# Optimization experiments

Hardware: AMD Instinct MI355X
Metric: run time of the kernel (lower is better)

The kernel has to match this reference:

```python
import jax, jax.numpy as jnp
import numpy as np

B, T, DIM = 2, 2048, 1024
H, DH, E, K = 16, 64, 8, 2


def setup_inputs() -> dict:
    key = jax.random.key(0)
    ks = jax.random.split(key, 7)
    s = 0.02
    return {
        "x":  jax.random.normal(ks[0], (B, T, DIM), jnp.float32),
        "Wq": jax.random.normal(ks[1], (H, DH, DIM), jnp.float32) * s,  # Linear(dim -> h*dh), reshaped
        "Wk": jax.random.normal(ks[2], (H, DH, DIM), jnp.float32) * s,
        "Wv": jax.random.normal(ks[3], (E, DH, DIM), jnp.float32) * s,  # per-expert Linear(dim -> dh)
        "Ws": jax.random.normal(ks[4], (H, E, DIM), jnp.float32) * s,   # V-gate Linear(dim -> h*e)
        "Wd": jax.random.normal(ks[5], (H, E, DIM), jnp.float32) * s,   # O-gate Linear(dim -> h*e)
        "Wo": jax.random.normal(ks[6], (E, DIM, DH), jnp.float32) * s,  # per-expert Linear(dh -> dim)
    }


def reference(x, Wq, Wk, Wv, Ws, Wd, Wo):
    scale = DH ** -0.5
    # projections: [b,h,t,dh]
    q = jnp.einsum('btc,hdc->bhtd', x, Wq)
    k = jnp.einsum('btc,hdc->bhtd', x, Wk)

    # ---- compute_moe (V experts): top-k gate, sigmoid weights ----
    gate_v = jnp.einsum('btc,hec->bthe', x, Ws)              # [b,t,h,e]
    w, sel = jax.lax.top_k(gate_v, K)                        # [b,t,h,K]
    wsig = jax.nn.sigmoid(w)
    oh = jax.nn.one_hot(sel, E, dtype=x.dtype)               # [b,t,h,K,e]
    mix_v = jnp.einsum('bthk,bthke->bthe', wsig, oh)         # weighted routing mask
    proj_v = jnp.einsum('btc,edc->bted', x, Wv)              # all-expert V projections (E small)
    v = jnp.einsum('bthe,bted->bhtd', mix_v, proj_v)         # [b,h,t,dh]

    # ---- standard attention core ----
    scores = jnp.einsum('bhid,bhjd->bhij', q * scale, k)     # [b,h,t,t]
    probs = jax.nn.softmax(scores, axis=-1)
    attn = jnp.einsum('bhij,bhjd->bihd', probs, v)           # [b,t,h,dh]

    # ---- compute_moe_o (O experts): top-k gate; NOTE original never uses its
    # softmax weights, so selected experts are summed UNWEIGHTED ----
    gate_o = jnp.einsum('btc,hec->bthe', x, Wd)
    _, sel_o = jax.lax.top_k(gate_o, K)
    mask_o = jax.nn.one_hot(sel_o, E, dtype=x.dtype).sum(axis=3)  # [b,t,h,e] in {0,1}
    res = jnp.einsum('bthe,bthd,efd->bthf', mask_o, attn, Wo)     # [b,t,h,dim]
    return res.sum(axis=2)                                        # [b,t,dim]
```

## Files before the change

kernel.cpp:

```cpp
#include <hip/hip_runtime.h>
#include <math.h>

#define TSEQ 2048
#define NB   2
#define NH   16
#define NE   8
#define DHD  64
#define MDIM 1024
#define MBT  4096
#define LDQKV 2560
#define GTAU 1e-3f
#define MAXFLAG 16384

typedef __attribute__((ext_vector_type(8))) short bf16x8;
typedef __attribute__((ext_vector_type(4))) float f32x4;
typedef __attribute__((ext_vector_type(16))) float f32x16;
typedef unsigned int u32;

__device__ inline unsigned short f2bf(float f) {
    union { float f; unsigned u; } v; v.f = f;
    unsigned r = v.u + 0x7fff + ((v.u >> 16) & 1);
    return (unsigned short)(r >> 16);
}
__device__ inline float bf2f(unsigned short h) {
    union { unsigned u; float f; } v; v.u = ((unsigned)h) << 16;
    return v.f;
}
__device__ inline u32 cvtpk(float a, float b) {
    u32 r;
    asm("v_cvt_pk_bf16_f32 %0, %1, %2" : "=v"(r) : "v"(a), "v"(b));
    return r;
}
__device__ inline float fexp2(float x) {
#if __has_builtin(__builtin_amdgcn_exp2f)
    return __builtin_amdgcn_exp2f(x);
#else
    float r; asm("v_exp_f32 %0, %1" : "=v"(r) : "v"(x)); return r;
#endif
}

__device__ inline void gload16(const void* g, void* l) {
    __builtin_amdgcn_global_load_lds((const __attribute__((address_space(1))) u32*)g,
                                     (__attribute__((address_space(3))) u32*)l, 16, 0, 0);
}

__device__ inline void cast8s(const float* __restrict__ in, unsigned short* __restrict__ out,
                              int i, float sc) {
    const float4* p = (const float4*)(in + (size_t)i * 8);
    float4 a = p[0], b = p[1];
    unsigned short o[8] = { f2bf(a.x*sc), f2bf(a.y*sc), f2bf(a.z*sc), f2bf(a.w*sc),
                            f2bf(b.x*sc), f2bf(b.y*sc), f2bf(b.z*sc), f2bf(b.w*sc) };
    *(uint4*)(out + (size_t)i * 8) = *(const uint4*)o;
}
__device__ inline void cast8hl(const float* __restrict__ in,
                               unsigned short* __restrict__ oh, unsigned short* __restrict__ ol,
                               int i) {
    const float4* p = (const float4*)(in + (size_t)i * 8);
    float4 a = p[0], b = p[1];
    float f[8] = { a.x, a.y, a.z, a.w, b.x, b.y, b.z, b.w };
    unsigned short h8[8], l8[8];
    #pragma unroll
    for (int j = 0; j < 8; ++j) {
        unsigned short hi = f2bf(f[j]);
        h8[j] = hi;
        l8[j] = f2bf(f[j] - bf2f(hi));
    }
    *(uint4*)(oh + (size_t)i * 8) = *(const uint4*)h8;
    *(uint4*)(ol + (size_t)i * 8) = *(const uint4*)l8;
}

__global__ __launch_bounds__(256)
void prep(const float* __restrict__ x,  const float* __restrict__ Wq,
          const float* __restrict__ Wk, const float* __restrict__ Wv,
          const float* __restrict__ Ws, const float* __restrict__ Wd,
          const float* __restrict__ Wo,
          unsigned short* __restrict__ xb, unsigned short* __restrict__ xbl,
          unsigned short* __restrict__ Wqkvb,
          unsigned short* __restrict__ Wsdh, unsigned short* __restrict__ Wsdl,
          unsigned short* __restrict__ WoTh, unsigned short* __restrict__ WoTl,
          u32* __restrict__ flags)
{
    const float qsc = 0.125f * 1.4426950408889634f;
    int b = blockIdx.x, tid = threadIdx.x;
    if (b == 0 && tid == 0) flags[0] = 0;
    if (b < 2048)      cast8hl(x, xb, xbl,          (b        ) * 256 + tid);
    else if (b < 2560) cast8s(Wq, Wqkvb,            (b - 2048) * 256 + tid, qsc);
    else if (b < 3072) cast8s(Wk, Wqkvb + 1048576,  (b - 2560) * 256 + tid, 1.f);
    else if (b < 3328) cast8s(Wv, Wqkvb + 2097152,  (b - 3072) * 256 + tid, 1.f);
    else if (b < 3456) {
        int i = (b - 3328) * 256 + tid;
        const float* src = (i < 16384) ? Ws + (size_t)i * 8 : Wd + (size_t)(i - 16384) * 8;
        const float4* p = (const float4*)src;
        float4 a = p[0], bq = p[1];
        float f8[8] = { a.x, a.y, a.z, a.w, bq.x, bq.y, bq.z, bq.w };
        unsigned short h8[8], l8[8];
        #pragma unroll
        for (int j = 0; j < 8; ++j) {
            unsigned short hi = f2bf(f8[j]);
            h8[j] = hi;
            l8[j] = f2bf(f8[j] - bf2f(hi));
        }
        *(uint4*)(Wsdh + (size_t)i * 8) = *(const uint4*)h8;
        *(uint4*)(Wsdl + (size_t)i * 8) = *(const uint4*)l8;
    } else {
        int idx = (b - 3456) * 256 + tid;
        int f = idx >> 9, ed = idx & 511, e = ed >> 6, d = ed & 63;
        float v = Wo[(size_t)e * (MDIM * DHD) + (size_t)f * DHD + d];
        unsigned short hi = f2bf(v);
        WoTh[idx] = hi;
        WoTl[idx] = f2bf(v - bf2f(hi));
    }
}

__global__ __launch_bounds__(256)
void qkvgate(const unsigned short* __restrict__ A,
             const unsigned short* __restrict__ B,
             unsigned short* __restrict__ C,
             const unsigned short* __restrict__ Al,
             const unsigned short* __restrict__ Bh2, const unsigned short* __restrict__ Bl2,
             float* __restrict__ Gf)
{
    __shared__ __align__(16) unsigned short S[8192];
    const int tid = threadIdx.x;
    const int lane = tid & 63, wave = tid >> 6;
    const int fr = lane & 15, fg = lane >> 4;
    const int grow = lane >> 2, gcol = (lane & 3) * 8;

    if (blockIdx.x < 640) {
        const int K = 1024, N = LDQKV, nbx = 20;
        unsigned short* As = S;
        unsigned short* Bs = S + 4096;
        const int o = blockIdx.x;
        const int virt = (o & 7) * 80 + (o >> 3);
        const int bx = virt % nbx, by = virt / nbx;
        const int m0 = by * 128, n0 = bx * 128;
        const int wm = (wave >> 1) * 64, wn = (wave & 1) * 64;

        f32x4 acc[4][4];
        #pragma unroll
        for (int i = 0; i < 4; ++i)
            #pragma unroll
            for (int j = 0; j < 4; ++j) acc[i][j] = (f32x4)0.f;

        for (int k0 = 0; k0 < K; k0 += 32) {
            __syncthreads();
            const unsigned short* gA = A + (size_t)(m0 + wave * 32 + grow) * K + k0 + gcol;
            gload16(gA,                  As + wave * 1024);
            gload16(gA + (size_t)16 * K, As + wave * 1024 + 512);
            const unsigned short* gB = B + (size_t)(n0 + wave * 32 + grow) * K + k0 + gcol;
            gload16(gB,                  Bs + wave * 1024);
            gload16(gB + (size_t)16 * K, Bs + wave * 1024 + 512);
            __syncthreads();
            bf16x8 af[4], bfr[4];
            #pragma unroll
            for (int t = 0; t < 4; ++t) {
                af[t]  = *(const bf16x8*)(As + (wm + t * 16 + fr) * 32 + fg * 8);
                bfr[t] = *(const bf16x8*)(Bs + (wn + t * 16 + fr) * 32 + fg * 8);
            }
            #pragma unroll
            for (int i = 0; i < 4; ++i)
                #pragma unroll
                for (int j = 0; j < 4; ++j)
                    acc[i][j] = __builtin_amdgcn_mfma_f32_16x16x32_bf16(af[i], bfr[j], acc[i][j], 0, 0, 0);
        }
        #pragma unroll
        for (int i = 0; i < 4; ++i)
            #pragma unroll
            for (int j = 0; j < 4; ++j)
                #pragma unroll
                for (int rr = 0; rr < 4; ++rr) {
                    int row = m0 + wm + i * 16 + fg * 4 + rr;
                    int col = n0 + wn + j * 16 + fr;
                    C[(size_t)row * N + col] = f2bf(acc[i][j][rr]);
                }
    } else {
        const int K = 1024, N = 256;
        const int g = blockIdx.x - 640;
        const int m0 = (g >> 2) * 64, n0 = (g & 3) * 64;
        const int wm = (wave >> 1) * 32, wn = (wave & 1) * 32;
        const unsigned short* src = (wave == 0) ? A : (wave == 1) ? Al : (wave == 2) ? Bh2 : Bl2;
        const int brow = (wave >= 2) ? n0 : m0;

        f32x4 acc[2][2];
        #pragma unroll
        for (int i = 0; i < 2; ++i)
            #pragma unroll
            for (int j = 0; j < 2; ++j) acc[i][j] = (f32x4)0.f;

        for (int k0 = 0; k0 < K; k0 += 32) {
            __syncthreads();
            #pragma unroll
            for (int i = 0; i < 4; ++i)
                gload16(src + (size_t)(brow + i * 16 + grow) * K + k0 + gcol,
                        S + wave * 2048 + i * 512);
            __syncthreads();
            bf16x8 ah[2], al[2], bh[2], bl[2];
            #pragma unroll
            for (int t = 0; t < 2; ++t) {
                ah[t] = *(const bf16x8*)(S +        (wm + t * 16 + fr) * 32 + fg * 8);
                al[t] = *(const bf16x8*)(S + 2048 + (wm + t * 16 + fr) * 32 + fg * 8);
                bh[t] = *(const bf16x8*)(S + 4096 + (wn + t * 16 + fr) * 32 + fg * 8);
                bl[t] = *(const bf16x8*)(S + 6144 + (wn + t * 16 + fr) * 32 + fg * 8);
            }
            #pragma unroll
            for (int i = 0; i < 2; ++i)
                #pragma unroll
                for (int j = 0; j < 2; ++j) {
                    acc[i][j] = __builtin_amdgcn_mfma_f32_16x16x32_bf16(ah[i], bh[j], acc[i][j], 0, 0, 0);
                    acc[i][j] = __builtin_amdgcn_mfma_f32_16x16x32_bf16(ah[i], bl[j], acc[i][j], 0, 0, 0);
                    acc[i][j] = __builtin_amdgcn_mfma_f32_16x16x32_bf16(al[i], bh[j], acc[i][j], 0, 0, 0);
                }
        }
        #pragma unroll
        for (int i = 0; i < 2; ++i)
            #pragma unroll
            for (int j = 0; j < 2; ++j)
                #pragma unroll
                for (int rr = 0; rr < 4; ++rr) {
                    int row = m0 + wm + i * 16 + fg * 4 + rr;
                    int col = n0 + wn + j * 16 + fr;
                    Gf[(size_t)row * N + col] = acc[i][j][rr];
                }
    }
}

__global__ __launch_bounds__(256)
void mfma_gemm3(const unsigned short* __restrict__ Ah, const unsigned short* __restrict__ Al,
                const unsigned short* __restrict__ Bh, const unsigned short* __restrict__ Bl,
                float* __restrict__ C)
{
    const int Kc = 512, N = 1024;
    __shared__ __align__(16) unsigned short Ash[128 * 32];
    __shared__ __align__(16) unsigned short Asl[128 * 32];
    __shared__ __align__(16) unsigned short Bsh[128 * 32];
    __shared__ __align__(16) unsigned short Bsl[128 * 32];
    const int o = blockIdx.x;
    const int virt = (o & 7) * 32 + (o >> 3);
    const int bx = virt & 7, by = virt >> 3;
    const int tid = threadIdx.x;
    const int lane = tid & 63, wave = tid >> 6;
    const int m0 = by * 128, n0 = bx * 128;
    const int wm = (wave >> 1) * 64, wn = (wave & 1) * 64;
    const int fr = lane & 15, fg = lane >> 4;
    const int grow = lane >> 2, gcol = (lane & 3) * 8;

    f32x4 acc[4][4];
    #pragma unroll
    for (int i = 0; i < 4; ++i)
        #pragma unroll
        for (int j = 0; j < 4; ++j) acc[i][j] = (f32x4)0.f;

    for (int k0 = 0; k0 < Kc; k0 += 32) {
        __syncthreads();
        const size_t roff  = (size_t)(m0 + wave * 32 + grow) * Kc + k0 + gcol;
        const size_t roffB = (size_t)(n0 + wave * 32 + grow) * Kc + k0 + gcol;
        gload16(Ah + roff,             Ash + wave * 1024);
        gload16(Ah + roff + 16 * Kc,   Ash + wave * 1024 + 512);
        gload16(Al + roff,             Asl + wave * 1024);
        gload16(Al + roff + 16 * Kc,   Asl + wave * 1024 + 512);
        gload16(Bh + roffB,            Bsh + wave * 1024);
        gload16(Bh + roffB + 16 * Kc,  Bsh + wave * 1024 + 512);
        gload16(Bl + roffB,            Bsl + wave * 1024);
        gload16(Bl + roffB + 16 * Kc,  Bsl + wave * 1024 + 512);
        __syncthreads();
        bf16x8 ah[4], al[4], bh[4], bl[4];
        #pragma unroll
        for (int t = 0; t < 4; ++t) {
            ah[t] = *(const bf16x8*)(Ash + (wm + t * 16 + fr) * 32 + fg * 8);
            al[t] = *(const bf16x8*)(Asl + (wm + t * 16 + fr) * 32 + fg * 8);
            bh[t] = *(const bf16x8*)(Bsh + (wn + t * 16 + fr) * 32 + fg * 8);
            bl[t] = *(const bf16x8*)(Bsl + (wn + t * 16 + fr) * 32 + fg * 8);
        }
        #pragma unroll
        for (int i = 0; i < 4; ++i)
            #pragma unroll
            for (int j = 0; j < 4; ++j) {
                acc[i][j] = __builtin_amdgcn_mfma_f32_16x16x32_bf16(ah[i], bh[j], acc[i][j], 0, 0, 0);
                acc[i][j] = __builtin_amdgcn_mfma_f32_16x16x32_bf16(ah[i], bl[j], acc[i][j], 0, 0, 0);
                acc[i][j] = __builtin_amdgcn_mfma_f32_16x16x32_bf16(al[i], bh[j], acc[i][j], 0, 0, 0);
            }
    }
    #pragma unroll
    for (int i = 0; i < 4; ++i)
        #pragma unroll
        for (int j = 0; j < 4; ++j)
            #pragma unroll
            for (int rr = 0; rr < 4; ++rr) {
                int row = m0 + wm + i * 16 + fg * 4 + rr;
                int col = n0 + wn + j * 16 + fr;
                C[(size_t)row * N + col] = acc[i][j][rr];
            }
}

__global__ __launch_bounds__(256)
void gate_topk2(const float* __restrict__ Gf,
                float2* __restrict__ wv, u32* __restrict__ selv, u32* __restrict__ selo,
                u32* __restrict__ flags)
{
    int item = blockIdx.x * 256 + threadIdx.x;
    int bt = item >> 4, h = item & 15;
    const float* g = Gf + (size_t)bt * 256 + h * NE;
    float b1 = -1e30f, b2 = -1e30f, b3 = -1e30f; int e1 = 0, e2 = 0;
    #pragma unroll
    for (int e = 0; e < NE; ++e) {
        float v = g[e];
        if (v > b1)      { b3 = b2; b2 = b1; e2 = e1; b1 = v; e1 = e; }
        else if (v > b2) { b3 = b2; b2 = v;  e2 = e; }
        else if (v > b3) { b3 = v; }
    }
    wv[item] = make_float2(1.f / (1.f + __expf(-b1)), 1.f / (1.f + __expf(-b2)));
    selv[item] = (u32)e1 | ((u32)e2 << 4);
    if (b2 - b3 < GTAU) {
        u32 p = atomicAdd(flags, 1u);
        if (p < MAXFLAG) flags[1 + p] = (u32)item;
    }
    const float* go = g + 128;
    float o1 = -1e30f, o2 = -1e30f, o3 = -1e30f; int f1 = 0, f2 = 0;
    #pragma unroll
    for (int e = 0; e < NE; ++e) {
        float v = go[e];
        if (v > o1)      { o3 = o2; o2 = o1; f2 = f1; o1 = v; f1 = e; }
        else if (v > o2) { o3 = o2; o2 = v;  f2 = e; }
        else if (v > o3) { o3 = v; }
    }
    selo[item] = (1u << f1) | (1u << f2);
    if (o2 - o3 < GTAU) {
        u32 p = atomicAdd(flags, 1u);
        if (p < MAXFLAG) flags[1 + p] = (u32)item | 0x10000u;
    }
}

__global__ __launch_bounds__(256)
void gate_fix(const float* __restrict__ x, const float* __restrict__ Ws,
              const float* __restrict__ Wd, const u32* __restrict__ flags,
              float2* __restrict__ wv, u32* __restrict__ selv, u32* __restrict__ selo)
{
    u32 nf = flags[0]; if (nf > MAXFLAG) nf = MAXFLAG;
    int gw = (blockIdx.x * 256 + threadIdx.x) >> 6;
    int lane = threadIdx.x & 63;
    int nwaves = gridDim.x * 4;
    for (u32 w = gw; w < nf; w += nwaves) {
        u32 rec = flags[1 + w];
        int item = rec & 0xffff, which = rec >> 16;
        int bt = item >> 4, h = item & 15;
        const float* W = (which ? Wd : Ws) + (size_t)h * NE * MDIM + lane * 16;
        const float* xr = x + (size_t)bt * MDIM + lane * 16;
        double g[8];
        #pragma unroll
        for (int e = 0; e < 8; ++e) {
            double s = 0.0;
            #pragma unroll
            for (int c = 0; c < 16; ++c)
                s += (double)xr[c] * (double)W[(size_t)e * MDIM + c];
            g[e] = s;
        }
        #pragma unroll
        for (int off = 32; off; off >>= 1)
            #pragma unroll
            for (int e = 0; e < 8; ++e)
                g[e] += __shfl_xor(g[e], off, 64);
        if (lane == 0) {
            double b1 = -1e300, b2 = -1e300; int i1 = 0, i2 = 0;
            #pragma unroll
            for (int e = 0; e < 8; ++e) {
                double v = g[e];
                if (v > b1)      { b2 = b1; i2 = i1; b1 = v; i1 = e; }
                else if (v > b2) { b2 = v;  i2 = e; }
            }
            if (which == 0) {
                wv[item] = make_float2(1.f / (1.f + __expf(-(float)b1)),
                                       1.f / (1.f + __expf(-(float)b2)));
                selv[item] = (u32)i1 | ((u32)i2 << 4);
            } else {
                selo[item] = (1u << i1) | (1u << i2);
            }
        }
    }
}

#define VTP 72
__global__ __launch_bounds__(256)
void vtrans(const unsigned short* __restrict__ QKVb, const float2* __restrict__ wv,
            const u32* __restrict__ selv, unsigned short* __restrict__ Vtg)
{
    __shared__ __align__(16) unsigned short Ls[256 * VTP];
    const int vid = blockIdx.x;
    const int xcd = vid & 7, local = vid >> 3;
    const int virt = xcd * 32 + local;
    const int b = virt >> 7, rem = virt & 127;
    const int tblk = rem >> 4, h = rem & 15;
    const int tid = threadIdx.x;

    {
        const int bt = b * TSEQ + tblk * 256 + tid;
        u32 s = selv[bt * 16 + h];
        float2 w = wv[bt * 16 + h];
        int e1 = s & 15, e2 = (s >> 4) & 15;
        const unsigned short* pv = QKVb + (size_t)bt * LDQKV + 2048;
        #pragma unroll
        for (int c = 0; c < 8; ++c) {
            uint4 a  = *(const uint4*)(pv + e1 * 64 + c * 8);
            uint4 bb = *(const uint4*)(pv + e2 * 64 + c * 8);
            unsigned short ea[8], eb[8], eo[8];
            *(uint4*)ea = a; *(uint4*)eb = bb;
            #pragma unroll
            for (int j = 0; j < 8; ++j)
                eo[j] = f2bf(w.x * bf2f(ea[j]) + w.y * bf2f(eb[j]));
            *(uint4*)(Ls + tid * VTP + c * 8) = *(const uint4*)eo;
        }
    }
    __syncthreads();
    {
        const int d = tid & 63, outer = tid >> 6;
        const size_t vrow = ((size_t)((b * NH + h) * DHD + d)) * TSEQ + tblk * 256;
        #pragma unroll
        for (int c8 = 0; c8 < 8; ++c8) {
            int t0 = (outer * 8 + c8) * 8;
            unsigned short o[8];
            #pragma unroll
            for (int j = 0; j < 8; ++j)
                o[j] = Ls[(t0 + j) * VTP + d];
            *(uint4*)(Vtg + vrow + t0) = *(const uint4*)o;
        }
    }
}

#define SPA 72
#define MFMA32(A,B,C) __builtin_amdgcn_mfma_f32_32x32x16_bf16(A, B, C, 0, 0, 0)
__global__ __launch_bounds__(256)
void attn_mfma(const unsigned short* __restrict__ QKVb,
               const unsigned short* __restrict__ Vtg,
               float* __restrict__ Op0, float* __restrict__ Op1,
               float* __restrict__ lp)
{
    __shared__ __align__(16) unsigned short Ks[64 * SPA];
    __shared__ __align__(16) unsigned short Vt[64 * SPA];
    const int vid = blockIdx.x;
    const int xcd = vid & 7, sl = vid >> 3;
    const int grp = xcd * 8 + (sl >> 4);
    const int q0  = (sl & 15) * 128;
    const int h   = grp & 15;
    const int z   = grp >> 4;
    const int b = z >> 1, split = z & 1;
    const int tid = threadIdx.x;
    const int lane = tid & 63, wq = tid >> 6;
    const int ql = lane & 31;
    const int hi = lane >> 5;
    const size_t base_q = ((size_t)b * TSEQ) * LDQKV + h * DHD;
    const size_t base_k = base_q + 1024;
    const size_t base_v = ((size_t)(b * NH + h) * DHD) * TSEQ;
    const int k00 = split * 1024;

    const int qrow = q0 + wq * 32 + ql;
    bf16x8 qa[4];
    #pragma unroll
    for (int t = 0; t < 4; ++t)
        qa[t] = *(const bf16x8*)(QKVb + base_q + (size_t)qrow * LDQKV + t * 16 + hi * 8);

    f32x16 o0 = (f32x16)0.f, o1 = (f32x16)0.f;
    float l_lane = 0.f;

    const int srow = tid >> 2, scol = (tid & 3) * 8;
    uint4 kr0 = *(const uint4*)(QKVb + base_k + (size_t)(k00 + srow) * LDQKV + scol);
    uint4 kr1 = *(const uint4*)(QKVb + base_k + (size_t)(k00 + srow) * LDQKV + scol + 32);
    uint4 vr0 = *(const uint4*)(Vtg + base_v + (size_t)srow * TSEQ + k00 + scol);
    uint4 vr1 = *(const uint4*)(Vtg + base_v + (size_t)srow * TSEQ + k00 + scol + 32);

    const int NT = 1024 / 64;
    for (int kb = 0; kb < NT; ++kb) {
        __syncthreads();
        *(uint4*)(Ks + srow * SPA + scol)      = kr0;
        *(uint4*)(Ks + srow * SPA + scol + 32) = kr1;
        *(uint4*)(Vt + srow * SPA + scol)      = vr0;
        *(uint4*)(Vt + srow * SPA + scol + 32) = vr1;
        __syncthreads();
        if (kb + 1 < NT) {
            const size_t gk = base_k + (size_t)(k00 + (kb + 1) * 64 + srow) * LDQKV + scol;
            const size_t gv = base_v + (size_t)srow * TSEQ + k00 + (kb + 1) * 64 + scol;
            kr0 = *(const uint4*)(QKVb + gk);
            kr1 = *(const uint4*)(QKVb + gk + 32);
            vr0 = *(const uint4*)(Vtg + gv);
            vr1 = *(const uint4*)(Vtg + gv + 32);
        }
        f32x16 s0 = (f32x16)0.f, s1 = (f32x16)0.f;
        #pragma unroll
        for (int t = 0; t < 4; ++t) {
            bf16x8 k0 = *(const bf16x8*)(Ks + ql * SPA + t * 16 + hi * 8);
            bf16x8 k1 = *(const bf16x8*)(Ks + (32 + ql) * SPA + t * 16 + hi * 8);
            s0 = MFMA32(k0, qa[t], s0);
            s1 = MFMA32(k1, qa[t], s1);
        }
        float ls0 = 0.f, ls1 = 0.f;
        u32 w[8];
        #pragma unroll
        for (int r = 0; r < 16; r += 2) {
            float pa = fexp2(s0[r]), pb = fexp2(s0[r + 1]);
            s0[r] = pa; s0[r + 1] = pb;
            ls0 += pa; ls1 += pb;
        }
        #pragma unroll
        for (int m = 0; m < 8; ++m) w[m] = cvtpk(s0[2*m], s0[2*m+1]);
        #pragma unroll
        for (int tl = 0; tl < 2; ++tl) {
            const int mb = 4 * tl, tk = tl;
            u32 send0 = hi ? w[mb]   : w[mb+2];
            u32 send1 = hi ? w[mb+1] : w[mb+3];
            u32 r0 = (u32)__shfl_xor((int)send0, 32, 64);
            u32 r1 = (u32)__shfl_xor((int)send1, 32, 64);
            union { u32 uw[4]; bf16x8 v; } pu;
            pu.uw[0] = hi ? r0 : w[mb];
            pu.uw[1] = hi ? r1 : w[mb+1];
            pu.uw[2] = hi ? w[mb+2] : r0;
            pu.uw[3] = hi ? w[mb+3] : r1;
            bf16x8 v0 = *(const bf16x8*)(Vt + ql * SPA + tk * 16 + hi * 8);
            bf16x8 v1 = *(const bf16x8*)(Vt + (32 + ql) * SPA + tk * 16 + hi * 8);
            o0 = MFMA32(pu.v, v0, o0);
            o1 = MFMA32(pu.v, v1, o1);
        }
        #pragma unroll
        for (int r = 0; r < 16; r += 2) {
            float pa = fexp2(s1[r]), pb = fexp2(s1[r + 1]);
            s1[r] = pa; s1[r + 1] = pb;
            ls0 += pa; ls1 += pb;
        }
        #pragma unroll
        for (int m = 0; m < 8; ++m) w[m] = cvtpk(s1[2*m], s1[2*m+1]);
        #pragma unroll
        for (int tl = 0; tl < 2; ++tl) {
            const int mb = 4 * tl, tk = 2 + tl;
            u32 send0 = hi ? w[mb]   : w[mb+2];
            u32 send1 = hi ? w[mb+1] : w[mb+3];
            u32 r0 = (u32)__shfl_xor((int)send0, 32, 64);
            u32 r1 = (u32)__shfl_xor((int)send1, 32, 64);
            union { u32 uw[4]; bf16x8 v; } pu;
            pu.uw[0] = hi ? r0 : w[mb];
            pu.uw[1] = hi ? r1 : w[mb+1];
            pu.uw[2] = hi ? w[mb+2] : r0;
            pu.uw[3] = hi ? w[mb+3] : r1;
            bf16x8 v0 = *(const bf16x8*)(Vt + ql * SPA + tk * 16 + hi * 8);
            bf16x8 v1 = *(const bf16x8*)(Vt + (32 + ql) * SPA + tk * 16 + hi * 8);
            o0 = MFMA32(pu.v, v0, o0);
            o1 = MFMA32(pu.v, v1, o1);
        }
        l_lane += ls0 + ls1;
    }
    float l_tot = l_lane + __shfl_xor(l_lane, 32, 64);
    float* Op = split ? Op1 : Op0;
    const size_t ob = ((size_t)b * TSEQ) * MDIM + h * DHD;
    #pragma unroll
    for (int r = 0; r < 16; ++r) {
        int qr = q0 + wq * 32 + (r & 3) + 8 * (r >> 2) + 4 * hi;
        Op[ob + (size_t)qr * MDIM + ql]      = o0[r];
        Op[ob + (size_t)qr * MDIM + 32 + ql] = o1[r];
    }
    if (hi == 0)
        lp[(((size_t)split * NB + b) * NH + h) * TSEQ + q0 + wq * 32 + ql] = l_tot;
}

__global__ __launch_bounds__(256)
void compute_U2(const float* __restrict__ Op0, const float* __restrict__ Op1,
                const float* __restrict__ lp, const u32* __restrict__ selo,
                unsigned short* __restrict__ Uh, unsigned short* __restrict__ Ul)
{
    int t = blockIdx.x * 256 + threadIdx.x;
    int bt = t >> 6, d = t & 63;
    int b = bt >> 11, ts = bt & 2047;
    float att[16];
    #pragma unroll
    for (int h = 0; h < NH; ++h) {
        size_t li = ((size_t)b * NH + h) * TSEQ + ts;
        float l = lp[li] + lp[li + (size_t)NB * NH * TSEQ];
        size_t oi = (size_t)bt * MDIM + h * DHD + d;
        att[h] = (Op0[oi] + Op1[oi]) / l;
    }
    const u32* sp = selo + bt * 16;
    u32 m[16];
    #pragma unroll
    for (int h = 0; h < NH; ++h) m[h] = sp[h];
    #pragma unroll
    for (int e = 0; e < NE; ++e) {
        float sum = 0.f;
        #pragma unroll
        for (int h = 0; h < NH; ++h)
            if (m[h] & (1u << e)) sum += att[h];
        int idx = bt * 512 + e * 64 + d;
        unsigned short hi16 = f2bf(sum);
        Uh[idx] = hi16;
        Ul[idx] = f2bf(sum - bf2f(hi16));
    }
}

extern "C" void kernel_launch(void* const* d_in, const int* in_sizes, int n_in,
                              void* d_out, int out_size, void* d_ws, size_t ws_size,
                              hipStream_t stream)
{
    const float* x  = (const float*)d_in[0];
    const float* Wq = (const float*)d_in[1];
    const float* Wk = (const float*)d_in[2];
    const float* Wv = (const float*)d_in[3];
    const float* Ws = (const float*)d_in[4];
    const float* Wd = (const float*)d_in[5];
    const float* Wo = (const float*)d_in[6];
    float* out = (float*)d_out;
    char* ws = (char*)d_ws;

    unsigned short* xb    = (unsigned short*)(ws);
    unsigned short* Wqkvb = (unsigned short*)(ws + 8388608);
    float*          Op0   = (float*)(ws);
    unsigned short* QKVb  = (unsigned short*)(ws + 16777216);
    unsigned short* Vtg   = (unsigned short*)(ws + 37748736);
    unsigned short* xbl   = (unsigned short*)(ws + 46137344);
    float*          Op1   = (float*)(ws + 46137344);
    float*          lp    = (float*)(ws + 62914560);
    unsigned short* WoTh  = (unsigned short*)(ws + 63438848);
    unsigned short* WoTl  = (unsigned short*)(ws + 64487424);
    float*          Gf    = (float*)(ws + 65536000);
    unsigned short* Uh    = (unsigned short*)(ws + 65536000);
    u32*            flags = (u32*)(ws + 69730304);
    unsigned short* Ul    = (unsigned short*)(ws + 69730304);
    float2*         wvp   = (float2*)(ws + 73924608);
    u32*            selv  = (u32*)(ws + 74448896);
    u32*            selo  = (u32*)(ws + 74711040);
    unsigned short* Wsdh  = (unsigned short*)(ws + 74973184);
    unsigned short* Wsdl  = (unsigned short*)(ws + 75497472);

    dim3 blk(256);
    prep<<<5504, blk, 0, stream>>>(x, Wq, Wk, Wv, Ws, Wd, Wo,
                                   xb, xbl, Wqkvb, Wsdh, Wsdl, WoTh, WoTl, flags);

    qkvgate<<<896, blk, 0, stream>>>(xb, Wqkvb, QKVb, xbl, Wsdh, Wsdl, Gf);

    gate_topk2<<<256, blk, 0, stream>>>(Gf, wvp, selv, selo, flags);
    gate_fix<<<128, blk, 0, stream>>>(x, Ws, Wd, flags, wvp, selv, selo);

    vtrans<<<256, blk, 0, stream>>>(QKVb, wvp, selv, Vtg);

    attn_mfma<<<1024, blk, 0, stream>>>(QKVb, Vtg, Op0, Op1, lp);

    compute_U2<<<1024, blk, 0, stream>>>(Op0, Op1, lp, selo, Uh, Ul);
    mfma_gemm3<<<256, blk, 0, stream>>>(Uh, Ul, WoTh, WoTl, out);
}
```

Measured before the change: 167.6 us.

## Fuse gate top-k into gate GEMM epilogue and halve output GEMM N-tile

The gate GEMM blocks inside qkvgate now stage their 64x64 fp32 tile in shared memory and run the top-2 expert selection, sigmoid weights and near-tie flagging directly. This removes the gate_topk2 launch and the Gf round trip through global memory. Separately, the final output GEMM uses 128x64 tiles instead of 128x128, doubling the grid to 512 blocks for better CU occupancy at the cost of reloading the A operand for twice as many tiles.

New measurement: 156.5 us. -6.6%, faster.

```diff
diff --git a/kernel.cpp b/kernel.cpp
--- a/kernel.cpp
+++ b/kernel.cpp
@@ -118,7 +118,8 @@
              unsigned short* __restrict__ C,
              const unsigned short* __restrict__ Al,
              const unsigned short* __restrict__ Bh2, const unsigned short* __restrict__ Bl2,
-             float* __restrict__ Gf)
+             float2* __restrict__ wv, u32* __restrict__ selv, u32* __restrict__ selo,
+             u32* __restrict__ flags)
 {
     __shared__ __align__(16) unsigned short S[8192];
     const int tid = threadIdx.x;
@@ -174,7 +175,7 @@
                     C[(size_t)row * N + col] = f2bf(acc[i][j][rr]);
                 }
     } else {
-        const int K = 1024, N = 256;
+        const int K = 1024;
         const int g = blockIdx.x - 640;
         const int m0 = (g >> 2) * 64, n0 = (g & 3) * 64;
         const int wm = (wave >> 1) * 32, wn = (wave & 1) * 32;
@@ -211,16 +212,47 @@
                     acc[i][j] = __builtin_amdgcn_mfma_f32_16x16x32_bf16(al[i], bh[j], acc[i][j], 0, 0, 0);
                 }
         }
+        float* Tf = (float*)S;
+        __syncthreads();
         #pragma unroll
         for (int i = 0; i < 2; ++i)
             #pragma unroll
             for (int j = 0; j < 2; ++j)
                 #pragma unroll
-                for (int rr = 0; rr < 4; ++rr) {
-                    int row = m0 + wm + i * 16 + fg * 4 + rr;
-                    int col = n0 + wn + j * 16 + fr;
-                    Gf[(size_t)row * N + col] = acc[i][j][rr];
+                for (int rr = 0; rr < 4; ++rr)
+                    Tf[(wm + i * 16 + fg * 4 + rr) * 64 + wn + j * 16 + fr] = acc[i][j][rr];
+        __syncthreads();
+        const int type = (n0 >= 128);
+        const int hbase = (n0 & 127) >> 3;
+        #pragma unroll
+        for (int k = 0; k < 2; ++k) {
+            int it = tid + k * 256;
+            int lr = it >> 3, lh = it & 7;
+            int item = (m0 + lr) * 16 + hbase + lh;
+            const float* gp = Tf + lr * 64 + lh * 8;
+            float b1 = -1e30f, b2 = -1e30f, b3 = -1e30f; int e1 = 0, e2 = 0;
+            #pragma unroll
+            for (int e = 0; e < NE; ++e) {
+                float v = gp[e];
+                if (v > b1)      { b3 = b2; b2 = b1; e2 = e1; b1 = v; e1 = e; }
+                else if (v > b2) { b3 = b2; b2 = v;  e2 = e; }
+                else if (v > b3) { b3 = v; }
+            }
+            if (type == 0) {
+                wv[item] = make_float2(1.f / (1.f + __expf(-b1)), 1.f / (1.f + __expf(-b2)));
+                selv[item] = (u32)e1 | ((u32)e2 << 4);
+                if (b2 - b3 < GTAU) {
+                    u32 p = atomicAdd(flags, 1u);
+                    if (p < MAXFLAG) flags[1 + p] = (u32)item;
                 }
+            } else {
+                selo[item] = (1u << e1) | (1u << e2);
+                if (b2 - b3 < GTAU) {
+                    u32 p = atomicAdd(flags, 1u);
+                    if (p < MAXFLAG) flags[1 + p] = (u32)item | 0x10000u;
+                }
+            }
+        }
     }
 }
 
@@ -232,49 +264,50 @@
     const int Kc = 512, N = 1024;
     __shared__ __align__(16) unsigned short Ash[128 * 32];
     __shared__ __align__(16) unsigned short Asl[128 * 32];
-    __shared__ __align__(16) unsigned short Bsh[128 * 32];
-    __shared__ __align__(16) unsigned short Bsl[128 * 32];
+    __shared__ __align__(16) unsigned short Bsh[64 * 32];
+    __shared__ __align__(16) unsigned short Bsl[64 * 32];
     const int o = blockIdx.x;
-    const int virt = (o & 7) * 32 + (o >> 3);
-    const int bx = virt & 7, by = virt >> 3;
+    const int virt = (o & 7) * 64 + (o >> 3);
+    const int bx = virt & 15, by = virt >> 4;
     const int tid = threadIdx.x;
     const int lane = tid & 63, wave = tid >> 6;
-    const int m0 = by * 128, n0 = bx * 128;
-    const int wm = (wave >> 1) * 64, wn = (wave & 1) * 64;
+    const int m0 = by * 128, n0 = bx * 64;
+    const int wm = (wave >> 1) * 64, wn = (wave & 1) * 32;
     const int fr = lane & 15, fg = lane >> 4;
     const int grow = lane >> 2, gcol = (lane & 3) * 8;
 
-    f32x4 acc[4][4];
+    f32x4 acc[4][2];
     #pragma unroll
     for (int i = 0; i < 4; ++i)
         #pragma unroll
-        for (int j = 0; j < 4; ++j) acc[i][j] = (f32x4)0.f;
+        for (int j = 0; j < 2; ++j) acc[i][j] = (f32x4)0.f;
 
     for (int k0 = 0; k0 < Kc; k0 += 32) {
         __syncthreads();
         const size_t roff  = (size_t)(m0 + wave * 32 + grow) * Kc + k0 + gcol;
-        const size_t roffB = (size_t)(n0 + wave * 32 + grow) * Kc + k0 + gcol;
+        const size_t roffB = (size_t)(n0 + wave * 16 + grow) * Kc + k0 + gcol;
         gload16(Ah + roff,             Ash + wave * 1024);
         gload16(Ah + roff + 16 * Kc,   Ash + wave * 1024 + 512);
         gload16(Al + roff,             Asl + wave * 1024);
         gload16(Al + roff + 16 * Kc,   Asl + wave * 1024 + 512);
-        gload16(Bh + roffB,            Bsh + wave * 1024);
-        gload16(Bh + roffB + 16 * Kc,  Bsh + wave * 1024 + 512);
-        gload16(Bl + roffB,            Bsl + wave * 1024);
-        gload16(Bl + roffB + 16 * Kc,  Bsl + wave * 1024 + 512);
+        gload16(Bh + roffB,            Bsh + wave * 512);
+        gload16(Bl + roffB,            Bsl + wave * 512);
         __syncthreads();
-        bf16x8 ah[4], al[4], bh[4], bl[4];
+        bf16x8 ah[4], al[4], bh[2], bl[2];
         #pragma unroll
         for (int t = 0; t < 4; ++t) {
             ah[t] = *(const bf16x8*)(Ash + (wm + t * 16 + fr) * 32 + fg * 8);
             al[t] = *(const bf16x8*)(Asl + (wm + t * 16 + fr) * 32 + fg * 8);
+        }
+        #pragma unroll
+        for (int t = 0; t < 2; ++t) {
             bh[t] = *(const bf16x8*)(Bsh + (wn + t * 16 + fr) * 32 + fg * 8);
             bl[t] = *(const bf16x8*)(Bsl + (wn + t * 16 + fr) * 32 + fg * 8);
         }
         #pragma unroll
         for (int i = 0; i < 4; ++i)
             #pragma unroll
-            for (int j = 0; j < 4; ++j) {
+            for (int j = 0; j < 2; ++j) {
                 acc[i][j] = __builtin_amdgcn_mfma_f32_16x16x32_bf16(ah[i], bh[j], acc[i][j], 0, 0, 0);
                 acc[i][j] = __builtin_amdgcn_mfma_f32_16x16x32_bf16(ah[i], bl[j], acc[i][j], 0, 0, 0);
                 acc[i][j] = __builtin_amdgcn_mfma_f32_16x16x32_bf16(al[i], bh[j], acc[i][j], 0, 0, 0);
@@ -283,51 +316,13 @@
     #pragma unroll
     for (int i = 0; i < 4; ++i)
         #pragma unroll
-        for (int j = 0; j < 4; ++j)
+        for (int j = 0; j < 2; ++j)
             #pragma unroll
             for (int rr = 0; rr < 4; ++rr) {
                 int row = m0 + wm + i * 16 + fg * 4 + rr;
                 int col = n0 + wn + j * 16 + fr;
                 C[(size_t)row * N + col] = acc[i][j][rr];
             }
-}
-
-__global__ __launch_bounds__(256)
-void gate_topk2(const float* __restrict__ Gf,
-                float2* __restrict__ wv, u32* __restrict__ selv, u32* __restrict__ selo,
-                u32* __restrict__ flags)
-{
-    int item = blockIdx.x * 256 + threadIdx.x;
-    int bt = item >> 4, h = item & 15;
-    const float* g = Gf + (size_t)bt * 256 + h * NE;
-    float b1 = -1e30f, b2 = -1e30f, b3 = -1e30f; int e1 = 0, e2 = 0;
-    #pragma unroll
-    for (int e = 0; e < NE; ++e) {
-        float v = g[e];
-        if (v > b1)      { b3 = b2; b2 = b1; e2 = e1; b1 = v; e1 = e; }
-        else if (v > b2) { b3 = b2; b2 = v;  e2 = e; }
-        else if (v > b3) { b3 = v; }
-    }
-    wv[item] = make_float2(1.f / (1.f + __expf(-b1)), 1.f / (1.f + __expf(-b2)));
-    selv[item] = (u32)e1 | ((u32)e2 << 4);
-    if (b2 - b3 < GTAU) {
-        u32 p = atomicAdd(flags, 1u);
-        if (p < MAXFLAG) flags[1 + p] = (u32)item;
-    }
-    const float* go = g + 128;
-    float o1 = -1e30f, o2 = -1e30f, o3 = -1e30f; int f1 = 0, f2 = 0;
-    #pragma unroll
-    for (int e = 0; e < NE; ++e) {
-        float v = go[e];
-        if (v > o1)      { o3 = o2; o2 = o1; f2 = f1; o1 = v; f1 = e; }
-        else if (v > o2) { o3 = o2; o2 = v;  f2 = e; }
-        else if (v > o3) { o3 = v; }
-    }
-    selo[item] = (1u << f1) | (1u << f2);
-    if (o2 - o3 < GTAU) {
-        u32 p = atomicAdd(flags, 1u);
-        if (p < MAXFLAG) flags[1 + p] = (u32)item | 0x10000u;
-    }
 }
 
 __global__ __launch_bounds__(256)
@@ -614,7 +609,6 @@
     float*          lp    = (float*)(ws + 62914560);
     unsigned short* WoTh  = (unsigned short*)(ws + 63438848);
     unsigned short* WoTl  = (unsigned short*)(ws + 64487424);
-    float*          Gf    = (float*)(ws + 65536000);
     unsigned short* Uh    = (unsigned short*)(ws + 65536000);
     u32*            flags = (u32*)(ws + 69730304);
     unsigned short* Ul    = (unsigned short*)(ws + 69730304);
@@ -628,9 +622,9 @@
     prep<<<5504, blk, 0, stream>>>(x, Wq, Wk, Wv, Ws, Wd, Wo,
                                    xb, xbl, Wqkvb, Wsdh, Wsdl, WoTh, WoTl, flags);
 
-    qkvgate<<<896, blk, 0, stream>>>(xb, Wqkvb, QKVb, xbl, Wsdh, Wsdl, Gf);
-
-    gate_topk2<<<256, blk, 0, stream>>>(Gf, wvp, selv, selo, flags);
+    qkvgate<<<896, blk, 0, stream>>>(xb, Wqkvb, QKVb, xbl, Wsdh, Wsdl,
+                                     wvp, selv, selo, flags);
+
     gate_fix<<<128, blk, 0, stream>>>(x, Ws, Wd, flags, wvp, selv, selo);
 
     vtrans<<<256, blk, 0, stream>>>(QKVb, wvp, selv, Vtg);
@@ -638,5 +632,5 @@
     attn_mfma<<<1024, blk, 0, stream>>>(QKVb, Vtg, Op0, Op1, lp);
 
     compute_U2<<<1024, blk, 0, stream>>>(Op0, Op1, lp, selo, Uh, Ul);
-    mfma_gemm3<<<256, blk, 0, stream>>>(Uh, Ul, WoTh, WoTl, out);
-}
+    mfma_gemm3<<<512, blk, 0, stream>>>(Uh, Ul, WoTh, WoTl, out);
+}
```
